# Kernel tuning notes

Hardware: AMD Instinct MI355X
Metric: run time of the kernel (lower is better)

The kernel has to match this reference:

```python
import jax, jax.numpy as jnp
import numpy as np

D_MODEL = 1024
N_HEADS = 16
D_HEAD = D_MODEL // N_HEADS
D_FF = 4096
B, S = 4, 1024
EPS = 1e-12


def layer_norm(x, gamma, beta):
    # Faithful to the torch module: unbiased std (ddof=1) and division by (std + eps).
    mean = jnp.mean(x, axis=-1, keepdims=True)
    var = jnp.sum((x - mean) ** 2, axis=-1, keepdims=True) / (x.shape[-1] - 1)
    std = jnp.sqrt(var)
    return gamma * (x - mean) / (std + EPS) + beta


def setup_inputs() -> dict:
    key = jax.random.key(0)
    ks = jax.random.split(key, 10)
    sc = lambda fan_in: 1.0 / np.sqrt(fan_in)
    inp = {
        "x": jax.random.normal(ks[0], (B, S, D_MODEL), dtype=jnp.float32),
        "ln1_g": jnp.ones((D_MODEL,), jnp.float32),
        "ln1_b": jnp.zeros((D_MODEL,), jnp.float32),
        "wq": jax.random.normal(ks[1], (D_MODEL, D_MODEL), jnp.float32) * sc(D_MODEL),
        "bq": jnp.zeros((D_MODEL,), jnp.float32),
        "wk": jax.random.normal(ks[2], (D_MODEL, D_MODEL), jnp.float32) * sc(D_MODEL),
        "bk": jnp.zeros((D_MODEL,), jnp.float32),
        "wv": jax.random.normal(ks[3], (D_MODEL, D_MODEL), jnp.float32) * sc(D_MODEL),
        "bv": jnp.zeros((D_MODEL,), jnp.float32),
        "ln2_g": jnp.ones((D_MODEL,), jnp.float32),
        "ln2_b": jnp.zeros((D_MODEL,), jnp.float32),
        "w1": jax.random.normal(ks[4], (D_FF, D_MODEL), jnp.float32) * sc(D_MODEL),
        "b1": jnp.zeros((D_FF,), jnp.float32),
        "w2": jax.random.normal(ks[5], (D_MODEL, D_FF), jnp.float32) * sc(D_FF),
        "b2": jnp.zeros((D_MODEL,), jnp.float32),
    }
    return inp


def reference(x, ln1_g, ln1_b, wq, bq, wk, bk, wv, bv, ln2_g, ln2_b, w1, b1, w2, b2):
    Bsz, Sq, D = x.shape
    residual = x
    h = layer_norm(x, ln1_g, ln1_b)
    # QKV projections (no output projection in the original module)
    q = (h @ wq.T + bq).reshape(Bsz, Sq, N_HEADS, D_HEAD)
    k = (h @ wk.T + bk).reshape(Bsz, Sq, N_HEADS, D_HEAD)
    v = (h @ wv.T + bv).reshape(Bsz, Sq, N_HEADS, D_HEAD)
    scores = jnp.einsum("bqhd,bkhd->bhqk", q, k) / np.sqrt(D_HEAD)
    attn = jax.nn.softmax(scores, axis=-1)  # [B, H, S, S]
    ctx = jnp.einsum("bhqk,bkhd->bqhd", attn, v).reshape(Bsz, Sq, D)
    out = ctx + residual
    residual = out
    h2 = layer_norm(out, ln2_g, ln2_b)
    # 1x1 conv FFN == per-token MLP with ReLU (dropout inactive at eval)
    ff = jax.nn.relu(h2 @ w1.T + b1) @ w2.T + b2
    out = ff + residual
    # torch returns attn flattened head-major: [H*B, S, S]
    attn_ret = jnp.transpose(attn, (1, 0, 2, 3)).reshape(N_HEADS * Bsz, Sq, Sq)
    return out, attn_ret
```

## Files before the change

kernel.cpp:

```cpp
#include <hip/hip_runtime.h>
#include <cstdint>
#include <cstddef>

#define SEQ 1024
#define DM 1024
#define DF 4096
#define NH 16
#define DH 64
#define BSZ 4
#define NTOK (BSZ*SEQ)
#define QKVSZ ((long)NTOK*DM)

typedef short s16x8 __attribute__((ext_vector_type(8)));
typedef float f32x4 __attribute__((ext_vector_type(4)));

__device__ __forceinline__ unsigned short f2bf(float f) {
  union { float f; unsigned u; } c; c.f = f;
  unsigned u = c.u;
  return (unsigned short)((u + 0x7fffu + ((u >> 16) & 1u)) >> 16);
}
__device__ __forceinline__ float bf2f(unsigned short b) {
  union { unsigned u; float f; } c; c.u = ((unsigned)b) << 16; return c.f;
}

__device__ __forceinline__ void gll16(const void* g, void* l) {
  __builtin_amdgcn_global_load_lds(
      (__attribute__((address_space(1))) void*)(g),
      (__attribute__((address_space(3))) void*)(l), 16, 0, 0);
}

template<int EPI>
__launch_bounds__(512, 2)
__global__ void gemm8_k(const unsigned short* __restrict__ A,
                        const unsigned short* __restrict__ W,
                        const float* __restrict__ bias,
                        void* __restrict__ outp,
                        int nNB, int K, int aRow, int wRow, int oRow,
                        float scale, long planeStride) {
  __shared__ __align__(16) char smem[131072];
  const int tid = threadIdx.x;
  const int kz = blockIdx.y;
  const int cpx = (int)gridDim.x >> 3;
  const int wgid = ((int)blockIdx.x & 7) * cpx + ((int)blockIdx.x >> 3);
  const int mb = wgid / nNB, nb = wgid % nNB;
  const unsigned short* Ag = A + (long)mb*256*aRow + (long)kz*K;
  const unsigned short* Wg = W + (long)nb*256*wRow + (long)kz*K;
  const int wave = tid >> 6, lane = tid & 63;
  const int quad = lane >> 4, l16 = lane & 15;
  const int wr = wave >> 2, wc = wave & 3;
  const int srow = tid >> 3, sch = tid & 7;
  const int swz = sch ^ (srow & 7);
  const int ldst = tid << 4;
  f32x4 acc[8][4] = {};

  auto stageA = [&](int q, int t, int buf) {
    gll16(Ag + (long)(q*64 + srow)*aRow + t*64 + swz*8,
          smem + buf*32768 + q*8192 + ldst);
  };
  auto stageB = [&](int q, int t, int buf) {
    gll16(Wg + (long)(q*64 + srow)*wRow + t*64 + swz*8,
          smem + 65536 + buf*32768 + q*8192 + ldst);
  };

  const int NTt = K >> 6;
  stageA(0,0,0); stageA(2,0,0); stageA(1,0,0); stageA(3,0,0);
  stageB(0,0,0); stageB(1,0,0); stageB(2,0,0); stageB(3,0,0);
  if (NTt > 1) {
    stageA(0,1,1); stageA(2,1,1);
    asm volatile("s_waitcnt vmcnt(2)" ::: "memory");
  } else {
    asm volatile("s_waitcnt vmcnt(0)" ::: "memory");
  }
  asm volatile("" ::: "memory"); __builtin_amdgcn_s_barrier();
  asm volatile("" ::: "memory");

  for (int t = 0; t < NTt; ++t) {
    const int cur = t & 1, nxt = cur ^ 1;
    const char* Ab = smem + cur*32768;
    const char* Bb = smem + 65536 + cur*32768;

#define G8_PHASE(MHF, NHF, STAGE_STMT, WAIT_STMT)                                \
    {                                                                            \
      s16x8 afr[4][2]; s16x8 bfr[2][2];                                          \
      _Pragma("unroll") for (int mf = 0; mf < 4; ++mf)                           \
      _Pragma("unroll") for (int ks = 0; ks < 2; ++ks) {                         \
        const int ra = wr*128 + MHF*64 + mf*16 + l16;                            \
        afr[mf][ks] = *(const s16x8*)(Ab + ra*128 + (((ks*4+quad)^(ra&7))<<4));  \
      }                                                                          \
      _Pragma("unroll") for (int nf = 0; nf < 2; ++nf)                           \
      _Pragma("unroll") for (int ks = 0; ks < 2; ++ks) {                         \
        const int rb = wc*64 + NHF*32 + nf*16 + l16;                             \
        bfr[nf][ks] = *(const s16x8*)(Bb + rb*128 + (((ks*4+quad)^(rb&7))<<4));  \
      }                                                                          \
      STAGE_STMT;                                                                \
      WAIT_STMT;                                                                 \
      asm volatile("" ::: "memory"); __builtin_amdgcn_s_barrier();               \
      asm volatile("" ::: "memory");                                             \
      __builtin_amdgcn_s_setprio(1);                                             \
      _Pragma("unroll") for (int nf = 0; nf < 2; ++nf)                           \
      _Pragma("unroll") for (int mf = 0; mf < 4; ++mf)                           \
      _Pragma("unroll") for (int ks = 0; ks < 2; ++ks)                           \
        acc[MHF*4+mf][NHF*2+nf] = __builtin_amdgcn_mfma_f32_16x16x32_bf16(       \
            afr[mf][ks], bfr[nf][ks], acc[MHF*4+mf][NHF*2+nf], 0, 0, 0);         \
      __builtin_amdgcn_s_setprio(0);                                             \
      asm volatile("" ::: "memory"); __builtin_amdgcn_s_barrier();               \
      asm volatile("" ::: "memory");                                             \
    }

    G8_PHASE(0, 0,
      if (t+1 < NTt) { stageA(1, t+1, nxt); stageA(3, t+1, nxt); }, )
    G8_PHASE(0, 1,
      if (t+1 < NTt) { stageB(0, t+1, nxt); stageB(1, t+1, nxt); }, )
    G8_PHASE(1, 0,
      if (t+1 < NTt) { stageB(2, t+1, nxt); stageB(3, t+1, nxt); }, )
    G8_PHASE(1, 1,
      if (t+2 < NTt) { stageA(0, t+2, cur); stageA(2, t+2, cur); },
      if (t+2 < NTt) { asm volatile("s_waitcnt vmcnt(2)" ::: "memory"); }
      else if (t+1 < NTt) { asm volatile("s_waitcnt vmcnt(0)" ::: "memory"); })
#undef G8_PHASE
  }

#pragma unroll
  for (int mt = 0; mt < 8; ++mt) {
#pragma unroll
    for (int nt = 0; nt < 4; ++nt) {
      const int gn = nb*256 + wc*64 + nt*16 + l16;
      const float bv = (EPI == 1 || EPI == 5) ? bias[gn] : 0.f;
      if (EPI == 5) {
        unsigned short* base = (unsigned short*)outp;
        const int reg = gn >> 10, cn = gn & 1023;
        if (reg == 2) {
          const int gm0 = mb*256 + wr*128 + mt*16 + quad*4;
          const int bb = gm0 >> 10, s0 = gm0 & 1023;
          ushort4 o4;
          o4.x = f2bf(acc[mt][nt][0] + bv);
          o4.y = f2bf(acc[mt][nt][1] + bv);
          o4.z = f2bf(acc[mt][nt][2] + bv);
          o4.w = f2bf(acc[mt][nt][3] + bv);
          *(ushort4*)&base[2*QKVSZ + (long)bb*DM*SEQ + (long)cn*SEQ + s0] = o4;
        } else {
#pragma unroll
          for (int r = 0; r < 4; ++r) {
            const int gm = mb*256 + wr*128 + mt*16 + quad*4 + r;
            const float v = acc[mt][nt][r] + bv;
            if (reg == 0) base[(long)gm*DM + cn] = f2bf(v * scale);
            else          base[QKVSZ + (long)gm*DM + cn] = f2bf(v);
          }
        }
      } else {
#pragma unroll
        for (int r = 0; r < 4; ++r) {
          const int gm = mb*256 + wr*128 + mt*16 + quad*4 + r;
          const float v = acc[mt][nt][r] + bv;
          if (EPI == 1) {
            ((unsigned short*)outp)[(long)gm*oRow + gn] = f2bf(v > 0.f ? v : 0.f);
          } else if (EPI == 7) {
            ((float*)outp)[(long)kz*planeStride + (long)gm*oRow + gn] = v;
          }
        }
      }
    }
  }
}

__launch_bounds__(256)
__global__ void comb_k(const float* __restrict__ p,
                       const float* __restrict__ b2,
                       const float* __restrict__ out1,
                       float* __restrict__ out) {
  const int i = blockIdx.x * 256 + threadIdx.x;
  const float4 a0 = ((const float4*)p)[i];
  const float4 a1 = ((const float4*)(p + (long)NTOK*DM))[i];
  const float4 a2 = ((const float4*)(p + 2L*NTOK*DM))[i];
  const float4 a3 = ((const float4*)(p + 3L*NTOK*DM))[i];
  const float4 bb = ((const float4*)b2)[i & (DM/4 - 1)];
  const float4 r = ((const float4*)out1)[i];
  float4 o;
  o.x = (a0.x + a1.x) + (a2.x + a3.x) + bb.x + r.x;
  o.y = (a0.y + a1.y) + (a2.y + a3.y) + bb.y + r.y;
  o.z = (a0.z + a1.z) + (a2.z + a3.z) + bb.z + r.z;
  o.w = (a0.w + a1.w) + (a2.w + a3.w) + bb.w + r.w;
  ((float4*)out)[i] = o;
}

__launch_bounds__(256)
__global__ void ln_k(const float* __restrict__ x, const float* __restrict__ g,
                     const float* __restrict__ bta, unsigned short* __restrict__ out) {
  const int row = blockIdx.x, t = threadIdx.x;
  const float4 v = ((const float4*)(x + (long)row*DM))[t];
  __shared__ float red[4];
  float s = v.x + v.y + v.z + v.w;
#pragma unroll
  for (int o = 32; o; o >>= 1) s += __shfl_down(s, o);
  if ((t & 63) == 0) red[t >> 6] = s;
  __syncthreads();
  const float mean = (red[0] + red[1] + red[2] + red[3]) * (1.f/1024.f);
  __syncthreads();
  const float dx = v.x - mean, dy = v.y - mean, dz = v.z - mean, dw = v.w - mean;
  float sq = dx*dx + dy*dy + dz*dz + dw*dw;
#pragma unroll
  for (int o = 32; o; o >>= 1) sq += __shfl_down(sq, o);
  if ((t & 63) == 0) red[t >> 6] = sq;
  __syncthreads();
  const float var = (red[0] + red[1] + red[2] + red[3]) * (1.f/1023.f);
  const float inv = 1.f / (sqrtf(var) + 1e-12f);
  const float4 gv = ((const float4*)g)[t];
  const float4 bv = ((const float4*)bta)[t];
  ushort4 o4;
  o4.x = f2bf(gv.x * dx * inv + bv.x);
  o4.y = f2bf(gv.y * dy * inv + bv.y);
  o4.z = f2bf(gv.z * dz * inv + bv.z);
  o4.w = f2bf(gv.w * dw * inv + bv.w);
  ((ushort4*)(out + (long)row*DM))[t] = o4;
}

#define R_WQ  262144L
#define R_WK  524288L
#define R_WV  786432L
#define R_W1  1835008L
#define R_W2  2883584L
#define CVT_BLOCKS 11265
__launch_bounds__(256)
__global__ void cvt5_k(const float* __restrict__ wq, const float* __restrict__ wk,
                       const float* __restrict__ wv, const float* __restrict__ w1,
                       const float* __restrict__ w2,
                       const float* __restrict__ bq, const float* __restrict__ bk,
                       const float* __restrict__ bvv,
                       unsigned short* __restrict__ wqkvb,
                       unsigned short* __restrict__ w1b,
                       unsigned short* __restrict__ w2b,
                       float* __restrict__ bcat) {
  const long blk = blockIdx.x;
  if (blk == CVT_BLOCKS - 1) {
    for (int j = threadIdx.x; j < 3072; j += 256)
      bcat[j] = j < 1024 ? bq[j] : (j < 2048 ? bk[j - 1024] : bvv[j - 2048]);
    return;
  }
  long i = blk*256 + threadIdx.x;
  const float* s; unsigned short* d;
  if (i < R_WQ)       { s = wq; d = wqkvb;              }
  else if (i < R_WK)  { s = wk; d = wqkvb + 1048576; i -= R_WQ; }
  else if (i < R_WV)  { s = wv; d = wqkvb + 2097152; i -= R_WK; }
  else if (i < R_W1)  { s = w1; d = w1b;             i -= R_WV; }
  else                { s = w2; d = w2b;             i -= R_W1; }
  const float4 v = ((const float4*)s)[i];
  ushort4 o; o.x = f2bf(v.x); o.y = f2bf(v.y); o.z = f2bf(v.z); o.w = f2bf(v.w);
  ((ushort4*)d)[i] = o;
}

#define LDP 1032
__launch_bounds__(256)
__global__ void attn_k(const unsigned short* __restrict__ Q,
                       const unsigned short* __restrict__ Kb,
                       const unsigned short* __restrict__ vt,
                       const float* __restrict__ xres,
                       float* __restrict__ attn_f,
                       float* __restrict__ out1) {
  const int b = blockIdx.y, h = blockIdx.z;
  const int q0 = blockIdx.x * 16;
  const int wave = threadIdx.x >> 6, lane = threadIdx.x & 63;
  const int quad = lane >> 4, l16 = lane & 15;
  __shared__ unsigned short PL[16 * LDP];
  __shared__ float red[4][16];

  const unsigned short* Qb = Q + (long)b*SEQ*DM + h*DH;
  const unsigned short* Kh = Kb + (long)b*SEQ*DM + h*DH;
  s16x8 af[2];
#pragma unroll
  for (int ks = 0; ks < 2; ++ks)
    af[ks] = *(const s16x8*)&Qb[(long)(q0 + l16)*DM + ks*32 + quad*8];
  f32x4 acc[16];
#pragma unroll
  for (int nt = 0; nt < 16; ++nt) acc[nt] = (f32x4){0.f, 0.f, 0.f, 0.f};
  for (int nt = 0; nt < 16; ++nt) {
    const int kc = wave*256 + nt*16 + l16;
#pragma unroll
    for (int ks = 0; ks < 2; ++ks) {
      const s16x8 bfr = *(const s16x8*)&Kh[(long)kc*DM + ks*32 + quad*8];
      acc[nt] = __builtin_amdgcn_mfma_f32_16x16x32_bf16(af[ks], bfr, acc[nt], 0, 0, 0);
    }
  }

  float rmax[4];
#pragma unroll
  for (int r = 0; r < 4; ++r) {
    float m = -3e38f;
#pragma unroll
    for (int nt = 0; nt < 16; ++nt) m = fmaxf(m, acc[nt][r]);
#pragma unroll
    for (int o = 1; o < 16; o <<= 1) m = fmaxf(m, __shfl_xor(m, o));
    rmax[r] = m;
  }
  if (l16 == 0) {
#pragma unroll
    for (int r = 0; r < 4; ++r) red[wave][quad*4 + r] = rmax[r];
  }
  __syncthreads();
#pragma unroll
  for (int r = 0; r < 4; ++r)
    rmax[r] = fmaxf(fmaxf(red[0][quad*4+r], red[1][quad*4+r]),
                    fmaxf(red[2][quad*4+r], red[3][quad*4+r]));
  __syncthreads();
#pragma unroll
  for (int r = 0; r < 4; ++r) {
    float s = 0.f;
#pragma unroll
    for (int nt = 0; nt < 16; ++nt) {
      const float e = __expf(acc[nt][r] - rmax[r]);
      acc[nt][r] = e; s += e;
    }
#pragma unroll
    for (int o = 1; o < 16; o <<= 1) s += __shfl_xor(s, o);
    if (l16 == 0) red[wave][quad*4 + r] = s;
  }
  __syncthreads();

  const long obase = (long)(h*BSZ + b)*SEQ*SEQ + (long)q0*SEQ;
#pragma unroll
  for (int r = 0; r < 4; ++r) {
    const float tot = red[0][quad*4+r] + red[1][quad*4+r] + red[2][quad*4+r] + red[3][quad*4+r];
    const float inv = 1.f / tot;
    unsigned short* prow = &PL[(quad*4 + r)*LDP + wave*256 + l16];
    float* arow = attn_f + obase + (long)(quad*4 + r)*SEQ + wave*256 + l16;
#pragma unroll
    for (int nt = 0; nt < 16; ++nt) {
      const float pv_ = acc[nt][r] * inv;
      prow[nt*16] = f2bf(pv_);
      arow[nt*16] = pv_;
    }
  }
  __syncthreads();

  f32x4 cc[4] = {};
  const unsigned short* Vh = vt + (long)b*DM*SEQ + (long)(h*DH + wave*16 + l16)*SEQ;
#pragma unroll
  for (int k0 = 0; k0 < 32; ++k0) {
    const s16x8 a  = *(const s16x8*)&PL[l16*LDP + k0*32 + quad*8];
    const s16x8 bf = *(const s16x8*)&Vh[k0*32 + quad*8];
    cc[k0 & 3] = __builtin_amdgcn_mfma_f32_16x16x32_bf16(a, bf, cc[k0 & 3], 0, 0, 0);
  }
  const f32x4 c = (cc[0] + cc[1]) + (cc[2] + cc[3]);

#pragma unroll
  for (int r = 0; r < 4; ++r) {
    const int gq = q0 + quad*4 + r;
    const int col = h*DH + wave*16 + l16;
    const long idx = (long)b*SEQ*DM + (long)gq*DM + col;
    out1[idx] = c[r] + xres[idx];
  }
}

extern "C" void kernel_launch(void* const* d_in, const int* in_sizes, int n_in,
                              void* d_out, int out_size, void* d_ws, size_t ws_size,
                              hipStream_t stream) {
  const float* x    = (const float*)d_in[0];
  const float* ln1g = (const float*)d_in[1];
  const float* ln1b = (const float*)d_in[2];
  const float* wq   = (const float*)d_in[3];
  const float* bq   = (const float*)d_in[4];
  const float* wk   = (const float*)d_in[5];
  const float* bk   = (const float*)d_in[6];
  const float* wv   = (const float*)d_in[7];
  const float* bv   = (const float*)d_in[8];
  const float* ln2g = (const float*)d_in[9];
  const float* ln2b = (const float*)d_in[10];
  const float* w1   = (const float*)d_in[11];
  const float* b1   = (const float*)d_in[12];
  const float* w2   = (const float*)d_in[13];
  const float* b2   = (const float*)d_in[14];
  float* out    = (float*)d_out;
  float* attn_f = out + (long)NTOK*DM;

  uint8_t* p = (uint8_t*)d_ws;
  auto alloc = [&](size_t bytes) {
    uint8_t* r = p; p += (bytes + 255) & ~(size_t)255; return r;
  };
  unsigned short* hbuf  = (unsigned short*)alloc((size_t)NTOK*DM*2);
  unsigned short* qkv   = (unsigned short*)alloc((size_t)3*NTOK*DM*2);
  unsigned short* h2    = (unsigned short*)alloc((size_t)NTOK*DM*2);
  unsigned short* f1    = (unsigned short*)alloc((size_t)NTOK*DF*2);
  float*          out1  = (float*)alloc((size_t)NTOK*DM*4);
  unsigned short* wqkvb = (unsigned short*)alloc((size_t)3*DM*DM*2);
  unsigned short* w1b   = (unsigned short*)alloc((size_t)DF*DM*2);
  unsigned short* w2b   = (unsigned short*)alloc((size_t)DM*DF*2);
  float*          bcat  = (float*)alloc((size_t)3*DM*4);
  float*          part  = (float*)alloc((size_t)4*NTOK*DM*4);

  cvt5_k<<<CVT_BLOCKS, 256, 0, stream>>>(wq, wk, wv, w1, w2, bq, bk, bv,
                                         wqkvb, w1b, w2b, bcat);
  ln_k<<<NTOK, 256, 0, stream>>>(x, ln1g, ln1b, hbuf);

  gemm8_k<5><<<dim3((NTOK/256)*(3*DM/256)), 512, 0, stream>>>(
      hbuf, wqkvb, bcat, qkv, 3*DM/256, DM, DM, DM, DM, 0.125f, 0);

  attn_k<<<dim3(SEQ/16, BSZ, NH), 256, 0, stream>>>(
      qkv, qkv + QKVSZ, qkv + 2*QKVSZ, x, attn_f, out1);

  ln_k<<<NTOK, 256, 0, stream>>>(out1, ln2g, ln2b, h2);

  gemm8_k<1><<<dim3((NTOK/256)*(DF/256)), 512, 0, stream>>>(
      h2, w1b, b1, f1, DF/256, DM, DM, DM, DF, 1.f, 0);

  gemm8_k<7><<<dim3((NTOK/256)*(DM/256), 4), 512, 0, stream>>>(
      f1, w2b, nullptr, part, DM/256, DF/4, DF, DF, DM, 1.f, (long)NTOK*DM);
  comb_k<<<(NTOK*DM)/1024, 256, 0, stream>>>(part, b2, out1, out);
}
```

Baseline: 611.6 us.

## Process 32 query rows per attention block and fold bias/residual into split-K GEMM

The attention kernel now handles 32 query rows per block instead of 16. Waves are split into two query groups and two key halves, so each K and V tile fetched from memory serves twice as many rows. This halves redundant K/V global traffic but doubles the score accumulators per thread (128 floats), which raises register pressure and may reduce occupancy. Separately, the FFN2 split-K GEMM adds b2 and the residual in its kz==0 slice, so the combine kernel no longer reads them.

```diff
diff --git a/kernel.cpp b/kernel.cpp
--- a/kernel.cpp
+++ b/kernel.cpp
@@ -35,6 +35,7 @@
                         const unsigned short* __restrict__ W,
                         const float* __restrict__ bias,
                         void* __restrict__ outp,
+                        const float* __restrict__ resid,
                         int nNB, int K, int aRow, int wRow, int oRow,
                         float scale, long planeStride) {
   __shared__ __align__(16) char smem[131072];
@@ -151,11 +152,13 @@
 #pragma unroll
         for (int r = 0; r < 4; ++r) {
           const int gm = mb*256 + wr*128 + mt*16 + quad*4 + r;
-          const float v = acc[mt][nt][r] + bv;
+          float v = acc[mt][nt][r] + bv;
           if (EPI == 1) {
             ((unsigned short*)outp)[(long)gm*oRow + gn] = f2bf(v > 0.f ? v : 0.f);
           } else if (EPI == 7) {
-            ((float*)outp)[(long)kz*planeStride + (long)gm*oRow + gn] = v;
+            const long o = (long)gm*oRow + gn;
+            if (kz == 0) v += bias[gn] + resid[o];
+            ((float*)outp)[(long)kz*planeStride + o] = v;
           }
         }
       }
@@ -165,21 +168,17 @@
 
 __launch_bounds__(256)
 __global__ void comb_k(const float* __restrict__ p,
-                       const float* __restrict__ b2,
-                       const float* __restrict__ out1,
                        float* __restrict__ out) {
   const int i = blockIdx.x * 256 + threadIdx.x;
   const float4 a0 = ((const float4*)p)[i];
   const float4 a1 = ((const float4*)(p + (long)NTOK*DM))[i];
   const float4 a2 = ((const float4*)(p + 2L*NTOK*DM))[i];
   const float4 a3 = ((const float4*)(p + 3L*NTOK*DM))[i];
-  const float4 bb = ((const float4*)b2)[i & (DM/4 - 1)];
-  const float4 r = ((const float4*)out1)[i];
   float4 o;
-  o.x = (a0.x + a1.x) + (a2.x + a3.x) + bb.x + r.x;
-  o.y = (a0.y + a1.y) + (a2.y + a3.y) + bb.y + r.y;
-  o.z = (a0.z + a1.z) + (a2.z + a3.z) + bb.z + r.z;
-  o.w = (a0.w + a1.w) + (a2.w + a3.w) + bb.w + r.w;
+  o.x = (a0.x + a1.x) + (a2.x + a3.x);
+  o.y = (a0.y + a1.y) + (a2.y + a3.y);
+  o.z = (a0.z + a1.z) + (a2.z + a3.z);
+  o.w = (a0.w + a1.w) + (a2.w + a3.w);
   ((float4*)out)[i] = o;
 }
 
@@ -257,23 +256,24 @@
                        float* __restrict__ attn_f,
                        float* __restrict__ out1) {
   const int b = blockIdx.y, h = blockIdx.z;
-  const int q0 = blockIdx.x * 16;
+  const int q0 = blockIdx.x * 32;
   const int wave = threadIdx.x >> 6, lane = threadIdx.x & 63;
   const int quad = lane >> 4, l16 = lane & 15;
-  __shared__ unsigned short PL[16 * LDP];
-  __shared__ float red[4][16];
+  const int qg = wave >> 1, cg = wave & 1;
+  __shared__ unsigned short PL[32 * LDP];
+  __shared__ float red[2][32];
 
   const unsigned short* Qb = Q + (long)b*SEQ*DM + h*DH;
   const unsigned short* Kh = Kb + (long)b*SEQ*DM + h*DH;
   s16x8 af[2];
 #pragma unroll
   for (int ks = 0; ks < 2; ++ks)
-    af[ks] = *(const s16x8*)&Qb[(long)(q0 + l16)*DM + ks*32 + quad*8];
-  f32x4 acc[16];
-#pragma unroll
-  for (int nt = 0; nt < 16; ++nt) acc[nt] = (f32x4){0.f, 0.f, 0.f, 0.f};
-  for (int nt = 0; nt < 16; ++nt) {
-    const int kc = wave*256 + nt*16 + l16;
+    af[ks] = *(const s16x8*)&Qb[(long)(q0 + qg*16 + l16)*DM + ks*32 + quad*8];
+  f32x4 acc[32];
+#pragma unroll
+  for (int nt = 0; nt < 32; ++nt) acc[nt] = (f32x4){0.f, 0.f, 0.f, 0.f};
+  for (int nt = 0; nt < 32; ++nt) {
+    const int kc = cg*512 + nt*16 + l16;
 #pragma unroll
     for (int ks = 0; ks < 2; ++ks) {
       const s16x8 bfr = *(const s16x8*)&Kh[(long)kc*DM + ks*32 + quad*8];
@@ -286,44 +286,46 @@
   for (int r = 0; r < 4; ++r) {
     float m = -3e38f;
 #pragma unroll
-    for (int nt = 0; nt < 16; ++nt) m = fmaxf(m, acc[nt][r]);
+    for (int nt = 0; nt < 32; ++nt) m = fmaxf(m, acc[nt][r]);
 #pragma unroll
     for (int o = 1; o < 16; o <<= 1) m = fmaxf(m, __shfl_xor(m, o));
     rmax[r] = m;
   }
   if (l16 == 0) {
 #pragma unroll
-    for (int r = 0; r < 4; ++r) red[wave][quad*4 + r] = rmax[r];
-  }
-  __syncthreads();
-#pragma unroll
-  for (int r = 0; r < 4; ++r)
-    rmax[r] = fmaxf(fmaxf(red[0][quad*4+r], red[1][quad*4+r]),
-                    fmaxf(red[2][quad*4+r], red[3][quad*4+r]));
+    for (int r = 0; r < 4; ++r) red[cg][qg*16 + quad*4 + r] = rmax[r];
+  }
+  __syncthreads();
+#pragma unroll
+  for (int r = 0; r < 4; ++r) {
+    const int row = qg*16 + quad*4 + r;
+    rmax[r] = fmaxf(red[0][row], red[1][row]);
+  }
   __syncthreads();
 #pragma unroll
   for (int r = 0; r < 4; ++r) {
     float s = 0.f;
 #pragma unroll
-    for (int nt = 0; nt < 16; ++nt) {
+    for (int nt = 0; nt < 32; ++nt) {
       const float e = __expf(acc[nt][r] - rmax[r]);
       acc[nt][r] = e; s += e;
     }
 #pragma unroll
     for (int o = 1; o < 16; o <<= 1) s += __shfl_xor(s, o);
-    if (l16 == 0) red[wave][quad*4 + r] = s;
+    if (l16 == 0) red[cg][qg*16 + quad*4 + r] = s;
   }
   __syncthreads();
 
   const long obase = (long)(h*BSZ + b)*SEQ*SEQ + (long)q0*SEQ;
 #pragma unroll
   for (int r = 0; r < 4; ++r) {
-    const float tot = red[0][quad*4+r] + red[1][quad*4+r] + red[2][quad*4+r] + red[3][quad*4+r];
+    const int row = qg*16 + quad*4 + r;
+    const float tot = red[0][row] + red[1][row];
     const float inv = 1.f / tot;
-    unsigned short* prow = &PL[(quad*4 + r)*LDP + wave*256 + l16];
-    float* arow = attn_f + obase + (long)(quad*4 + r)*SEQ + wave*256 + l16;
-#pragma unroll
-    for (int nt = 0; nt < 16; ++nt) {
+    unsigned short* prow = &PL[row*LDP + cg*512 + l16];
+    float* arow = attn_f + obase + (long)row*SEQ + cg*512 + l16;
+#pragma unroll
+    for (int nt = 0; nt < 32; ++nt) {
       const float pv_ = acc[nt][r] * inv;
       prow[nt*16] = f2bf(pv_);
       arow[nt*16] = pv_;
@@ -331,22 +333,26 @@
   }
   __syncthreads();
 
-  f32x4 cc[4] = {};
   const unsigned short* Vh = vt + (long)b*DM*SEQ + (long)(h*DH + wave*16 + l16)*SEQ;
+  f32x4 cc0[4] = {}, cc1[4] = {};
 #pragma unroll
   for (int k0 = 0; k0 < 32; ++k0) {
-    const s16x8 a  = *(const s16x8*)&PL[l16*LDP + k0*32 + quad*8];
     const s16x8 bf = *(const s16x8*)&Vh[k0*32 + quad*8];
-    cc[k0 & 3] = __builtin_amdgcn_mfma_f32_16x16x32_bf16(a, bf, cc[k0 & 3], 0, 0, 0);
-  }
-  const f32x4 c = (cc[0] + cc[1]) + (cc[2] + cc[3]);
+    const s16x8 a0 = *(const s16x8*)&PL[(l16)*LDP + k0*32 + quad*8];
+    const s16x8 a1 = *(const s16x8*)&PL[(16 + l16)*LDP + k0*32 + quad*8];
+    cc0[k0 & 3] = __builtin_amdgcn_mfma_f32_16x16x32_bf16(a0, bf, cc0[k0 & 3], 0, 0, 0);
+    cc1[k0 & 3] = __builtin_amdgcn_mfma_f32_16x16x32_bf16(a1, bf, cc1[k0 & 3], 0, 0, 0);
+  }
+  const f32x4 c0 = (cc0[0] + cc0[1]) + (cc0[2] + cc0[3]);
+  const f32x4 c1 = (cc1[0] + cc1[1]) + (cc1[2] + cc1[3]);
 
 #pragma unroll
   for (int r = 0; r < 4; ++r) {
-    const int gq = q0 + quad*4 + r;
     const int col = h*DH + wave*16 + l16;
-    const long idx = (long)b*SEQ*DM + (long)gq*DM + col;
-    out1[idx] = c[r] + xres[idx];
+    const long i0 = (long)b*SEQ*DM + (long)(q0 + quad*4 + r)*DM + col;
+    out1[i0] = c0[r] + xres[i0];
+    const long i1 = (long)b*SEQ*DM + (long)(q0 + 16 + quad*4 + r)*DM + col;
+    out1[i1] = c1[r] + xres[i1];
   }
 }
 
@@ -391,17 +397,17 @@
   ln_k<<<NTOK, 256, 0, stream>>>(x, ln1g, ln1b, hbuf);
 
   gemm8_k<5><<<dim3((NTOK/256)*(3*DM/256)), 512, 0, stream>>>(
-      hbuf, wqkvb, bcat, qkv, 3*DM/256, DM, DM, DM, DM, 0.125f, 0);
-
-  attn_k<<<dim3(SEQ/16, BSZ, NH), 256, 0, stream>>>(
+      hbuf, wqkvb, bcat, qkv, nullptr, 3*DM/256, DM, DM, DM, DM, 0.125f, 0);
+
+  attn_k<<<dim3(SEQ/32, BSZ, NH), 256, 0, stream>>>(
       qkv, qkv + QKVSZ, qkv + 2*QKVSZ, x, attn_f, out1);
 
   ln_k<<<NTOK, 256, 0, stream>>>(out1, ln2g, ln2b, h2);
 
   gemm8_k<1><<<dim3((NTOK/256)*(DF/256)), 512, 0, stream>>>(
-      h2, w1b, b1, f1, DF/256, DM, DM, DM, DF, 1.f, 0);
+      h2, w1b, b1, f1, nullptr, DF/256, DM, DM, DM, DF, 1.f, 0);
 
   gemm8_k<7><<<dim3((NTOK/256)*(DM/256), 4), 512, 0, stream>>>(
-      f1, w2b, nullptr, part, DM/256, DF/4, DF, DF, DM, 1.f, (long)NTOK*DM);
-  comb_k<<<(NTOK*DM)/1024, 256, 0, stream>>>(part, b2, out1, out);
-}
+      f1, w2b, b2, part, out1, DM/256, DF/4, DF, DF, DM, 1.f, (long)NTOK*DM);
+  comb_k<<<(NTOK*DM)/1024, 256, 0, stream>>>(part, out);
+}
```

New measurement: 680.8 us. 1.11x slower.

## Coalesce attention-probability stores via LDS and fold bias/residual into split-K GEMM

Applied to the files above, without the earlier changes.

The attention kernel no longer writes fp32 probabilities with strided scalar stores. It now rereads the bf16 probability tile from LDS after the PV product and writes each row as contiguous float4 stores. This also means the returned attention matrix carries bf16-rounded values, which costs precision. The residual load for the attention output is issued before the PV MFMA loop so its latency overlaps the math. The FFN2 split-K GEMM now adds bias and residual in its kz==0 plane, so the combine kernel reads only the four partial planes.

```diff
diff --git a/kernel.cpp b/kernel.cpp
--- a/kernel.cpp
+++ b/kernel.cpp
@@ -35,6 +35,7 @@
                         const unsigned short* __restrict__ W,
                         const float* __restrict__ bias,
                         void* __restrict__ outp,
+                        const float* __restrict__ resid,
                         int nNB, int K, int aRow, int wRow, int oRow,
                         float scale, long planeStride) {
   __shared__ __align__(16) char smem[131072];
@@ -151,11 +152,13 @@
 #pragma unroll
         for (int r = 0; r < 4; ++r) {
           const int gm = mb*256 + wr*128 + mt*16 + quad*4 + r;
-          const float v = acc[mt][nt][r] + bv;
+          float v = acc[mt][nt][r] + bv;
           if (EPI == 1) {
             ((unsigned short*)outp)[(long)gm*oRow + gn] = f2bf(v > 0.f ? v : 0.f);
           } else if (EPI == 7) {
-            ((float*)outp)[(long)kz*planeStride + (long)gm*oRow + gn] = v;
+            const long o = (long)gm*oRow + gn;
+            if (kz == 0) v += bias[gn] + resid[o];
+            ((float*)outp)[(long)kz*planeStride + o] = v;
           }
         }
       }
@@ -165,21 +168,17 @@
 
 __launch_bounds__(256)
 __global__ void comb_k(const float* __restrict__ p,
-                       const float* __restrict__ b2,
-                       const float* __restrict__ out1,
                        float* __restrict__ out) {
   const int i = blockIdx.x * 256 + threadIdx.x;
   const float4 a0 = ((const float4*)p)[i];
   const float4 a1 = ((const float4*)(p + (long)NTOK*DM))[i];
   const float4 a2 = ((const float4*)(p + 2L*NTOK*DM))[i];
   const float4 a3 = ((const float4*)(p + 3L*NTOK*DM))[i];
-  const float4 bb = ((const float4*)b2)[i & (DM/4 - 1)];
-  const float4 r = ((const float4*)out1)[i];
   float4 o;
-  o.x = (a0.x + a1.x) + (a2.x + a3.x) + bb.x + r.x;
-  o.y = (a0.y + a1.y) + (a2.y + a3.y) + bb.y + r.y;
-  o.z = (a0.z + a1.z) + (a2.z + a3.z) + bb.z + r.z;
-  o.w = (a0.w + a1.w) + (a2.w + a3.w) + bb.w + r.w;
+  o.x = (a0.x + a1.x) + (a2.x + a3.x);
+  o.y = (a0.y + a1.y) + (a2.y + a3.y);
+  o.z = (a0.z + a1.z) + (a2.z + a3.z);
+  o.w = (a0.w + a1.w) + (a2.w + a3.w);
   ((float4*)out)[i] = o;
 }
 
@@ -315,21 +314,22 @@
   }
   __syncthreads();
 
-  const long obase = (long)(h*BSZ + b)*SEQ*SEQ + (long)q0*SEQ;
 #pragma unroll
   for (int r = 0; r < 4; ++r) {
     const float tot = red[0][quad*4+r] + red[1][quad*4+r] + red[2][quad*4+r] + red[3][quad*4+r];
     const float inv = 1.f / tot;
     unsigned short* prow = &PL[(quad*4 + r)*LDP + wave*256 + l16];
-    float* arow = attn_f + obase + (long)(quad*4 + r)*SEQ + wave*256 + l16;
-#pragma unroll
-    for (int nt = 0; nt < 16; ++nt) {
-      const float pv_ = acc[nt][r] * inv;
-      prow[nt*16] = f2bf(pv_);
-      arow[nt*16] = pv_;
-    }
-  }
-  __syncthreads();
+#pragma unroll
+    for (int nt = 0; nt < 16; ++nt)
+      prow[nt*16] = f2bf(acc[nt][r] * inv);
+  }
+  __syncthreads();
+
+  float xr[4];
+  const int ocol = h*DH + wave*16 + l16;
+#pragma unroll
+  for (int r = 0; r < 4; ++r)
+    xr[r] = xres[(long)b*SEQ*DM + (long)(q0 + quad*4 + r)*DM + ocol];
 
   f32x4 cc[4] = {};
   const unsigned short* Vh = vt + (long)b*DM*SEQ + (long)(h*DH + wave*16 + l16)*SEQ;
@@ -343,10 +343,20 @@
 
 #pragma unroll
   for (int r = 0; r < 4; ++r) {
-    const int gq = q0 + quad*4 + r;
-    const int col = h*DH + wave*16 + l16;
-    const long idx = (long)b*SEQ*DM + (long)gq*DM + col;
-    out1[idx] = c[r] + xres[idx];
+    const long idx = (long)b*SEQ*DM + (long)(q0 + quad*4 + r)*DM + ocol;
+    out1[idx] = c[r] + xr[r];
+  }
+
+  {
+    const long obase = (long)(h*BSZ + b)*SEQ*SEQ + (long)q0*SEQ;
+    const int col = threadIdx.x * 4;
+#pragma unroll
+    for (int row = 0; row < 16; ++row) {
+      const ushort4 pv = *(const ushort4*)&PL[row*LDP + col];
+      float4 o;
+      o.x = bf2f(pv.x); o.y = bf2f(pv.y); o.z = bf2f(pv.z); o.w = bf2f(pv.w);
+      ((float4*)(attn_f + obase + (long)row*SEQ))[threadIdx.x] = o;
+    }
   }
 }
 
@@ -391,7 +401,7 @@
   ln_k<<<NTOK, 256, 0, stream>>>(x, ln1g, ln1b, hbuf);
 
   gemm8_k<5><<<dim3((NTOK/256)*(3*DM/256)), 512, 0, stream>>>(
-      hbuf, wqkvb, bcat, qkv, 3*DM/256, DM, DM, DM, DM, 0.125f, 0);
+      hbuf, wqkvb, bcat, qkv, nullptr, 3*DM/256, DM, DM, DM, DM, 0.125f, 0);
 
   attn_k<<<dim3(SEQ/16, BSZ, NH), 256, 0, stream>>>(
       qkv, qkv + QKVSZ, qkv + 2*QKVSZ, x, attn_f, out1);
@@ -399,9 +409,9 @@
   ln_k<<<NTOK, 256, 0, stream>>>(out1, ln2g, ln2b, h2);
 
   gemm8_k<1><<<dim3((NTOK/256)*(DF/256)), 512, 0, stream>>>(
-      h2, w1b, b1, f1, DF/256, DM, DM, DM, DF, 1.f, 0);
+      h2, w1b, b1, f1, nullptr, DF/256, DM, DM, DM, DF, 1.f, 0);
 
   gemm8_k<7><<<dim3((NTOK/256)*(DM/256), 4), 512, 0, stream>>>(
-      f1, w2b, nullptr, part, DM/256, DF/4, DF, DF, DM, 1.f, (long)NTOK*DM);
-  comb_k<<<(NTOK*DM)/1024, 256, 0, stream>>>(part, b2, out1, out);
-}
+      f1, w2b, b2, part, out1, DM/256, DF/4, DF, DF, DM, 1.f, (long)NTOK*DM);
+  comb_k<<<(NTOK*DM)/1024, 256, 0, stream>>>(part, out);
+}
```

New measurement: 642.0 us. +5.0%, slower.
